# Kernel tuning notes

Measured on AMD Instinct MI355X. Metric: run time of the kernel, lower is better.

The kernel has to match this reference:

```python
import jax, jax.numpy as jnp
import numpy as np

S, T, BERT, POS = 256, 512, 768, 128
H1 = 1024
NUM_CLASSES = 6


def setup_inputs() -> dict:
    key = jax.random.key(0)
    ks = jax.random.split(key, 12)
    emb = jax.random.normal(ks[0], (S, T, BERT), dtype=jnp.float32)
    pos = jax.random.normal(ks[1], (S, T, POS), dtype=jnp.float32)
    seg = jnp.sort(jax.random.randint(ks[2], (S,), 0, 64)).astype(jnp.int32)
    scale = 0.02
    return {
        "embeddings": emb,
        "position_encodings": pos,
        "W_attn": jax.random.normal(ks[3], (BERT + POS, 1), dtype=jnp.float32) * scale,
        "b_attn": jnp.zeros((1,), dtype=jnp.float32),
        "W1": jax.random.normal(ks[4], (BERT, H1), dtype=jnp.float32) * scale,
        "b1": jnp.zeros((H1,), dtype=jnp.float32),
        "W2": jax.random.normal(ks[5], (H1, H1), dtype=jnp.float32) * scale,
        "b2": jnp.zeros((H1,), dtype=jnp.float32),
        "W3": jax.random.normal(ks[6], (H1, NUM_CLASSES), dtype=jnp.float32) * scale,
        "b3": jnp.zeros((NUM_CLASSES,), dtype=jnp.float32),
        "segment_ids": seg,
        "num_comments": 64,
    }


def reference(embeddings, position_encodings, W_attn, b_attn, W1, b1, W2, b2, W3, b3, segment_ids, num_comments):
    # attention logits: Linear(bert+pos -> 1) over concatenated features, shape (S, T, 1)
    attn = jnp.concatenate([embeddings, position_encodings], axis=2) @ W_attn + b_attn
    # per-segment softmax over the 512-token dim (torch Softmax(1) on (b-a, 512, 1))
    w = jax.nn.softmax(attn, axis=1)
    # softmax-weighted pooling per segment -> (S, BERT)
    segvec = jnp.sum(w * embeddings, axis=1)
    # ragged sum over each comment's segments (contiguous bounds == sorted segment ids)
    vecs = jax.ops.segment_sum(segvec, segment_ids, num_segments=num_comments)
    # MLP head with LeakyReLU (torch default slope 0.01) and Sigmoid
    h = jax.nn.leaky_relu(vecs @ W1 + b1, negative_slope=0.01)
    h = jax.nn.leaky_relu(h @ W2 + b2, negative_slope=0.01)
    return jax.nn.sigmoid(h @ W3 + b3)
```

## Files before the change

### kernel.cpp

```cpp
#include <hip/hip_runtime.h>
#include <math.h>

#define S_SEQ 256
#define T_TOK 512
#define BERT 768
#define POSD 128
#define H1 1024
#define NC 6

#define HALF_T 256
#define TILE_T 16
#define NTILES (HALF_T / TILE_T)

__global__ __launch_bounds__(256, 2) void pool_kernel(
    const float* __restrict__ emb, const float* __restrict__ pos,
    const float* __restrict__ Wa, const float* __restrict__ ba,
    float* __restrict__ part_acc, float* __restrict__ part_ml)
{
    __shared__ float lds_tile[TILE_T * BERT];
    __shared__ float lds_plog[HALF_T];
    __shared__ float lds_logit[TILE_T];

    const int tid  = threadIdx.x;
    const int wave = tid >> 6;
    const int lane = tid & 63;
    const int b    = blockIdx.x;
    const int s    = b >> 1;
    const int t0   = (b & 1) * HALF_T;

    const float4* Wa4 = (const float4*)Wa;
    float4 wa_e[3];
    wa_e[0] = Wa4[lane];
    wa_e[1] = Wa4[64 + lane];
    wa_e[2] = Wa4[128 + lane];
    const int lane32 = lane & 31;
    const int half32 = lane >> 5;
    const float4 wp = Wa4[192 + lane32];
    const float bav = ba[0];

    const float4* pos4 = (const float4*)pos;
    #pragma unroll 4
    for (int it = 0; it < 32; ++it) {
        const int tl = wave * 64 + it * 2 + half32;
        const size_t gi = ((size_t)s * T_TOK + (t0 + tl)) * (POSD/4) + lane32;
        const float4 p = pos4[gi];
        float d = p.x*wp.x + p.y*wp.y + p.z*wp.z + p.w*wp.w;
        #pragma unroll
        for (int off = 16; off >= 1; off >>= 1) d += __shfl_xor(d, off, 32);
        if (lane32 == 0) lds_plog[tl] = d + bav;
    }

    float m = -INFINITY;
    float l = 0.f;
    float acc0 = 0.f, acc1 = 0.f, acc2 = 0.f;

    const float4* emb_blk4 =
        (const float4*)(emb + ((size_t)s * T_TOK + t0) * BERT);
    float4* lds4 = (float4*)lds_tile;

    for (int tt = 0; tt < NTILES; ++tt) {
        __syncthreads();

        {
            const float4* src = emb_blk4 + (size_t)tt * (TILE_T*BERT/4);
            float4 tmp[12];
            #pragma unroll
            for (int i = 0; i < 12; ++i) tmp[i] = src[i*256 + tid];
            #pragma unroll
            for (int i = 0; i < 12; ++i) lds4[i*256 + tid] = tmp[i];
        }
        __syncthreads();

        #pragma unroll
        for (int q = 0; q < 4; ++q) {
            const int t = wave * 4 + q;
            const float4* row4 = (const float4*)&lds_tile[t * BERT];
            float d = 0.f;
            #pragma unroll
            for (int i = 0; i < 3; ++i) {
                const float4 v = row4[i*64 + lane];
                d += v.x*wa_e[i].x + v.y*wa_e[i].y + v.z*wa_e[i].z + v.w*wa_e[i].w;
            }
            #pragma unroll
            for (int off = 32; off >= 1; off >>= 1) d += __shfl_xor(d, off, 64);
            if (lane == 0) lds_logit[t] = d + lds_plog[tt*TILE_T + t];
        }
        __syncthreads();

        float tmax = lds_logit[0];
        #pragma unroll
        for (int t = 1; t < TILE_T; ++t) tmax = fmaxf(tmax, lds_logit[t]);
        const float m_new = fmaxf(m, tmax);
        const float alpha = __expf(m - m_new);
        float p[TILE_T];
        float psum = 0.f;
        #pragma unroll
        for (int t = 0; t < TILE_T; ++t) {
            p[t] = __expf(lds_logit[t] - m_new);
            psum += p[t];
        }
        l = l * alpha + psum;
        acc0 *= alpha; acc1 *= alpha; acc2 *= alpha;
        #pragma unroll
        for (int t = 0; t < TILE_T; ++t) {
            acc0 = fmaf(p[t], lds_tile[t*BERT +       tid], acc0);
            acc1 = fmaf(p[t], lds_tile[t*BERT + 256 + tid], acc1);
            acc2 = fmaf(p[t], lds_tile[t*BERT + 512 + tid], acc2);
        }
        m = m_new;
    }

    part_acc[(size_t)b*BERT +       tid] = acc0;
    part_acc[(size_t)b*BERT + 256 + tid] = acc1;
    part_acc[(size_t)b*BERT + 512 + tid] = acc2;
    if (tid == 0) { part_ml[b*2] = m; part_ml[b*2+1] = l; }
}

__global__ void combine_segsum(
    const float* __restrict__ part_acc, const float* __restrict__ part_ml,
    const int* __restrict__ seg, float* __restrict__ vecs)
{
    const int c = blockIdx.x;
    const int tid = threadIdx.x;
    float v0 = 0.f, v1 = 0.f, v2 = 0.f;
    for (int s = 0; s < S_SEQ; ++s) {
        if (seg[s] != c) continue;
        const int p0 = 2*s, p1 = 2*s + 1;
        const float m0 = part_ml[p0*2], l0 = part_ml[p0*2+1];
        const float m1 = part_ml[p1*2], l1 = part_ml[p1*2+1];
        const float M  = fmaxf(m0, m1);
        const float e0 = __expf(m0 - M), e1 = __expf(m1 - M);
        const float inv = 1.0f / (l0*e0 + l1*e1);
        const float a = e0 * inv, bb = e1 * inv;
        v0 += a*part_acc[(size_t)p0*BERT +       tid] + bb*part_acc[(size_t)p1*BERT +       tid];
        v1 += a*part_acc[(size_t)p0*BERT + 256 + tid] + bb*part_acc[(size_t)p1*BERT + 256 + tid];
        v2 += a*part_acc[(size_t)p0*BERT + 512 + tid] + bb*part_acc[(size_t)p1*BERT + 512 + tid];
    }
    vecs[(size_t)c*BERT +       tid] = v0;
    vecs[(size_t)c*BERT + 256 + tid] = v1;
    vecs[(size_t)c*BERT + 512 + tid] = v2;
}

__global__ void mlp_layer(
    const float* __restrict__ in, const float* __restrict__ W,
    const float* __restrict__ bias, float* __restrict__ out, int K)
{
    __shared__ float v[H1];
    const int c  = blockIdx.y;
    const int tid = threadIdx.x;
    const int j  = blockIdx.x * 256 + tid;
    for (int i = tid; i < K; i += 256) v[i] = in[(size_t)c*K + i];
    __syncthreads();
    float a0 = 0.f, a1 = 0.f, a2 = 0.f, a3 = 0.f;
    #pragma unroll 4
    for (int k = 0; k < K; k += 4) {
        a0 = fmaf(v[k  ], W[(size_t)(k  )*H1 + j], a0);
        a1 = fmaf(v[k+1], W[(size_t)(k+1)*H1 + j], a1);
        a2 = fmaf(v[k+2], W[(size_t)(k+2)*H1 + j], a2);
        a3 = fmaf(v[k+3], W[(size_t)(k+3)*H1 + j], a3);
    }
    const float acc = bias[j] + ((a0 + a1) + (a2 + a3));
    out[(size_t)c*H1 + j] = acc > 0.f ? acc : 0.01f * acc;
}

__global__ void mlp_out(
    const float* __restrict__ h, const float* __restrict__ W3,
    const float* __restrict__ b3, float* __restrict__ out)
{
    __shared__ float v[H1];
    __shared__ float red[NC][4];
    const int c = blockIdx.x;
    const int tid = threadIdx.x;
    const int wave = tid >> 6, lane = tid & 63;
    for (int i = tid; i < H1; i += 256) v[i] = h[(size_t)c*H1 + i];
    __syncthreads();
    float po[NC] = {0.f, 0.f, 0.f, 0.f, 0.f, 0.f};
    for (int k = tid; k < H1; k += 256) {
        const float hv = v[k];
        #pragma unroll
        for (int o = 0; o < NC; ++o) po[o] = fmaf(hv, W3[k*NC + o], po[o]);
    }
    #pragma unroll
    for (int o = 0; o < NC; ++o) {
        float d = po[o];
        #pragma unroll
        for (int off = 32; off >= 1; off >>= 1) d += __shfl_xor(d, off, 64);
        if (lane == 0) red[o][wave] = d;
    }
    __syncthreads();
    if (tid < NC) {
        const float sum = red[tid][0] + red[tid][1] + red[tid][2] + red[tid][3] + b3[tid];
        out[c*NC + tid] = 1.0f / (1.0f + __expf(-sum));
    }
}

extern "C" void kernel_launch(void* const* d_in, const int* in_sizes, int n_in,
                              void* d_out, int out_size, void* d_ws, size_t ws_size,
                              hipStream_t stream)
{
    const float* emb = (const float*)d_in[0];
    const float* pos = (const float*)d_in[1];
    const float* Wa  = (const float*)d_in[2];
    const float* ba  = (const float*)d_in[3];
    const float* W1  = (const float*)d_in[4];
    const float* b1  = (const float*)d_in[5];
    const float* W2  = (const float*)d_in[6];
    const float* b2  = (const float*)d_in[7];
    const float* W3  = (const float*)d_in[8];
    const float* b3  = (const float*)d_in[9];
    const int*   seg = (const int*)d_in[10];
    float* out = (float*)d_out;

    float* ws = (float*)d_ws;
    float* part_acc = ws;
    float* part_ml  = part_acc + 512*BERT;
    float* vecs     = part_ml  + 512*2;
    float* h1       = vecs     + 64*BERT;
    float* h2       = h1       + 64*H1;

    pool_kernel<<<512, 256, 0, stream>>>(emb, pos, Wa, ba, part_acc, part_ml);
    combine_segsum<<<64, 256, 0, stream>>>(part_acc, part_ml, seg, vecs);
    mlp_layer<<<dim3(4, 64), 256, 0, stream>>>(vecs, W1, b1, h1, BERT);
    mlp_layer<<<dim3(4, 64), 256, 0, stream>>>(h1, W2, b2, h2, H1);
    mlp_out<<<64, 256, 0, stream>>>(h2, W3, b3, out);
}
```

Before: 684.3 us.

## Double-buffer async LDS loads in pooling and batch comments in MLP layers

The pooling kernel splits each sequence into four 128-token chunks and streams 8-token tiles into LDS with async global-to-LDS loads, double-buffered so the next tile loads while the current one is processed. Each wave owns two tokens per tile and keeps per-lane accumulators, and an online-softmax merge across waves replaces the per-tile block barriers and serial logit scan. The combine step is updated to merge four partials per sequence. The MLP layers now process four comments per block so each weight load is reused four times. Costs include more partial traffic and possible LDS bank conflicts from the strided per-lane row reads.

Measured after the change: 812.2 us. 18.7% more time.

```diff
diff --git a/kernel.cpp b/kernel.cpp
--- a/kernel.cpp
+++ b/kernel.cpp
@@ -1,5 +1,6 @@
 #include <hip/hip_runtime.h>
 #include <math.h>
+#include <stdint.h>
 
 #define S_SEQ 256
 #define T_TOK 512
@@ -8,112 +9,139 @@
 #define H1 1024
 #define NC 6
 
-#define HALF_T 256
-#define TILE_T 16
-#define NTILES (HALF_T / TILE_T)
-
-__global__ __launch_bounds__(256, 2) void pool_kernel(
+#define CHUNK_T 128
+#define TILE_T 8
+#define NTILES (CHUNK_T / TILE_T)
+#define TILE_FLOATS (TILE_T * BERT)
+
+__device__ __forceinline__ void async_load16(const float* g, float* lds_uniform) {
+    auto* l3 = reinterpret_cast<__attribute__((address_space(3))) uint32_t*>(
+        reinterpret_cast<uintptr_t>(lds_uniform));
+    auto* g1 = reinterpret_cast<const __attribute__((address_space(1))) uint32_t*>(
+        reinterpret_cast<uintptr_t>(g));
+    __builtin_amdgcn_global_load_lds(g1, l3, 16, 0, 0);
+}
+
+__global__ __launch_bounds__(256, 3) void pool_kernel(
     const float* __restrict__ emb, const float* __restrict__ pos,
     const float* __restrict__ Wa, const float* __restrict__ ba,
     float* __restrict__ part_acc, float* __restrict__ part_ml)
 {
-    __shared__ float lds_tile[TILE_T * BERT];
-    __shared__ float lds_plog[HALF_T];
-    __shared__ float lds_logit[TILE_T];
-
-    const int tid  = threadIdx.x;
-    const int wave = tid >> 6;
-    const int lane = tid & 63;
-    const int b    = blockIdx.x;
-    const int s    = b >> 1;
-    const int t0   = (b & 1) * HALF_T;
+    __shared__ float smem[2 * TILE_FLOATS + CHUNK_T + 8];
+    float* plog = smem + 2 * TILE_FLOATS;
+    float* wml  = plog + CHUNK_T;
+
+    const int tid = threadIdx.x;
+    const int w   = tid >> 6;
+    const int l   = tid & 63;
+    const int b   = blockIdx.x;
+    const int s   = b >> 2;
+    const int t0  = (b & 3) * CHUNK_T;
+
+    const float* gbase = emb + ((size_t)s * T_TOK + t0) * BERT;
+
+    #pragma unroll
+    for (int c = 0; c < 6; ++c)
+        async_load16(gbase + (w * 6 + c) * 256 + l * 4, smem + (w * 6 + c) * 256);
 
     const float4* Wa4 = (const float4*)Wa;
-    float4 wa_e[3];
-    wa_e[0] = Wa4[lane];
-    wa_e[1] = Wa4[64 + lane];
-    wa_e[2] = Wa4[128 + lane];
-    const int lane32 = lane & 31;
-    const int half32 = lane >> 5;
-    const float4 wp = Wa4[192 + lane32];
+    const float4 wa0 = Wa4[l * 3 + 0];
+    const float4 wa1 = Wa4[l * 3 + 1];
+    const float4 wa2 = Wa4[l * 3 + 2];
+    const int l32 = l & 31;
+    const float4 wp = Wa4[192 + l32];
     const float bav = ba[0];
 
     const float4* pos4 = (const float4*)pos;
-    #pragma unroll 4
-    for (int it = 0; it < 32; ++it) {
-        const int tl = wave * 64 + it * 2 + half32;
-        const size_t gi = ((size_t)s * T_TOK + (t0 + tl)) * (POSD/4) + lane32;
-        const float4 p = pos4[gi];
-        float d = p.x*wp.x + p.y*wp.y + p.z*wp.z + p.w*wp.w;
+    const int hw = tid >> 5;
+    for (int it = 0; it < CHUNK_T / 8; ++it) {
+        const int tl = it * 8 + hw;
+        const float4 p = pos4[((size_t)s * T_TOK + t0 + tl) * (POSD / 4) + l32];
+        float d = p.x * wp.x + p.y * wp.y + p.z * wp.z + p.w * wp.w;
         #pragma unroll
         for (int off = 16; off >= 1; off >>= 1) d += __shfl_xor(d, off, 32);
-        if (lane32 == 0) lds_plog[tl] = d + bav;
-    }
-
-    float m = -INFINITY;
-    float l = 0.f;
-    float acc0 = 0.f, acc1 = 0.f, acc2 = 0.f;
-
-    const float4* emb_blk4 =
-        (const float4*)(emb + ((size_t)s * T_TOK + t0) * BERT);
-    float4* lds4 = (float4*)lds_tile;
+        if (l32 == 0) plog[tl] = d + bav;
+    }
+
+    float m = -INFINITY, lsum = 0.f;
+    float acc[12];
+    #pragma unroll
+    for (int j = 0; j < 12; ++j) acc[j] = 0.f;
 
     for (int tt = 0; tt < NTILES; ++tt) {
+        float* cur = smem + (tt & 1) * TILE_FLOATS;
         __syncthreads();
 
-        {
-            const float4* src = emb_blk4 + (size_t)tt * (TILE_T*BERT/4);
-            float4 tmp[12];
+        if (tt + 1 < NTILES) {
+            float* nxt = smem + ((tt + 1) & 1) * TILE_FLOATS;
+            const float* src = gbase + (size_t)(tt + 1) * TILE_FLOATS;
             #pragma unroll
-            for (int i = 0; i < 12; ++i) tmp[i] = src[i*256 + tid];
-            #pragma unroll
-            for (int i = 0; i < 12; ++i) lds4[i*256 + tid] = tmp[i];
+            for (int c = 0; c < 6; ++c)
+                async_load16(src + (w * 6 + c) * 256 + l * 4, nxt + (w * 6 + c) * 256);
         }
-        __syncthreads();
-
-        #pragma unroll
-        for (int q = 0; q < 4; ++q) {
-            const int t = wave * 4 + q;
-            const float4* row4 = (const float4*)&lds_tile[t * BERT];
-            float d = 0.f;
-            #pragma unroll
-            for (int i = 0; i < 3; ++i) {
-                const float4 v = row4[i*64 + lane];
-                d += v.x*wa_e[i].x + v.y*wa_e[i].y + v.z*wa_e[i].z + v.w*wa_e[i].w;
-            }
-            #pragma unroll
-            for (int off = 32; off >= 1; off >>= 1) d += __shfl_xor(d, off, 64);
-            if (lane == 0) lds_logit[t] = d + lds_plog[tt*TILE_T + t];
+
+        const int i0 = tt * TILE_T + w * 2;
+        const float4* r0 = (const float4*)(cur + (w * 2) * BERT);
+        const float4* r1 = (const float4*)(cur + (w * 2 + 1) * BERT);
+        const float4 a0 = r0[l * 3 + 0], a1 = r0[l * 3 + 1], a2 = r0[l * 3 + 2];
+        const float4 b0 = r1[l * 3 + 0], b1 = r1[l * 3 + 1], b2 = r1[l * 3 + 2];
+
+        float d0 = a0.x*wa0.x + a0.y*wa0.y + a0.z*wa0.z + a0.w*wa0.w
+                 + a1.x*wa1.x + a1.y*wa1.y + a1.z*wa1.z + a1.w*wa1.w
+                 + a2.x*wa2.x + a2.y*wa2.y + a2.z*wa2.z + a2.w*wa2.w;
+        float d1 = b0.x*wa0.x + b0.y*wa0.y + b0.z*wa0.z + b0.w*wa0.w
+                 + b1.x*wa1.x + b1.y*wa1.y + b1.z*wa1.z + b1.w*wa1.w
+                 + b2.x*wa2.x + b2.y*wa2.y + b2.z*wa2.z + b2.w*wa2.w;
+        #pragma unroll
+        for (int off = 32; off >= 1; off >>= 1) {
+            d0 += __shfl_xor(d0, off, 64);
+            d1 += __shfl_xor(d1, off, 64);
         }
-        __syncthreads();
-
-        float tmax = lds_logit[0];
-        #pragma unroll
-        for (int t = 1; t < TILE_T; ++t) tmax = fmaxf(tmax, lds_logit[t]);
-        const float m_new = fmaxf(m, tmax);
-        const float alpha = __expf(m - m_new);
-        float p[TILE_T];
-        float psum = 0.f;
-        #pragma unroll
-        for (int t = 0; t < TILE_T; ++t) {
-            p[t] = __expf(lds_logit[t] - m_new);
-            psum += p[t];
-        }
-        l = l * alpha + psum;
-        acc0 *= alpha; acc1 *= alpha; acc2 *= alpha;
-        #pragma unroll
-        for (int t = 0; t < TILE_T; ++t) {
-            acc0 = fmaf(p[t], lds_tile[t*BERT +       tid], acc0);
-            acc1 = fmaf(p[t], lds_tile[t*BERT + 256 + tid], acc1);
-            acc2 = fmaf(p[t], lds_tile[t*BERT + 512 + tid], acc2);
-        }
-        m = m_new;
-    }
-
-    part_acc[(size_t)b*BERT +       tid] = acc0;
-    part_acc[(size_t)b*BERT + 256 + tid] = acc1;
-    part_acc[(size_t)b*BERT + 512 + tid] = acc2;
-    if (tid == 0) { part_ml[b*2] = m; part_ml[b*2+1] = l; }
+
+        const float lg0 = d0 + plog[i0];
+        const float lg1 = d1 + plog[i0 + 1];
+        const float mn = fmaxf(m, fmaxf(lg0, lg1));
+        const float alpha = __expf(m - mn);
+        const float p0 = __expf(lg0 - mn);
+        const float p1 = __expf(lg1 - mn);
+        lsum = lsum * alpha + p0 + p1;
+        m = mn;
+
+        acc[0]  = fmaf(p0, a0.x, fmaf(p1, b0.x, acc[0]  * alpha));
+        acc[1]  = fmaf(p0, a0.y, fmaf(p1, b0.y, acc[1]  * alpha));
+        acc[2]  = fmaf(p0, a0.z, fmaf(p1, b0.z, acc[2]  * alpha));
+        acc[3]  = fmaf(p0, a0.w, fmaf(p1, b0.w, acc[3]  * alpha));
+        acc[4]  = fmaf(p0, a1.x, fmaf(p1, b1.x, acc[4]  * alpha));
+        acc[5]  = fmaf(p0, a1.y, fmaf(p1, b1.y, acc[5]  * alpha));
+        acc[6]  = fmaf(p0, a1.z, fmaf(p1, b1.z, acc[6]  * alpha));
+        acc[7]  = fmaf(p0, a1.w, fmaf(p1, b1.w, acc[7]  * alpha));
+        acc[8]  = fmaf(p0, a2.x, fmaf(p1, b2.x, acc[8]  * alpha));
+        acc[9]  = fmaf(p0, a2.y, fmaf(p1, b2.y, acc[9]  * alpha));
+        acc[10] = fmaf(p0, a2.z, fmaf(p1, b2.z, acc[10] * alpha));
+        acc[11] = fmaf(p0, a2.w, fmaf(p1, b2.w, acc[11] * alpha));
+    }
+
+    __syncthreads();
+    float* mg = smem;
+    #pragma unroll
+    for (int j = 0; j < 12; ++j) mg[w * BERT + l * 12 + j] = acc[j];
+    if (l == 0) { wml[w * 2] = m; wml[w * 2 + 1] = lsum; }
+    __syncthreads();
+
+    const float m0 = wml[0], l0 = wml[1], m1 = wml[2], l1 = wml[3];
+    const float m2 = wml[4], l2 = wml[5], m3 = wml[6], l3 = wml[7];
+    const float M  = fmaxf(fmaxf(m0, m1), fmaxf(m2, m3));
+    const float e0 = __expf(m0 - M), e1 = __expf(m1 - M);
+    const float e2 = __expf(m2 - M), e3 = __expf(m3 - M);
+    const float lt = l0 * e0 + l1 * e1 + l2 * e2 + l3 * e3;
+    #pragma unroll
+    for (int k = 0; k < 3; ++k) {
+        const int col = tid * 3 + k;
+        const float v = e0 * mg[col] + e1 * mg[BERT + col]
+                      + e2 * mg[2 * BERT + col] + e3 * mg[3 * BERT + col];
+        part_acc[(size_t)b * BERT + col] = v;
+    }
+    if (tid == 0) { part_ml[b * 2] = M; part_ml[b * 2 + 1] = lt; }
 }
 
 __global__ void combine_segsum(
@@ -125,42 +153,59 @@
     float v0 = 0.f, v1 = 0.f, v2 = 0.f;
     for (int s = 0; s < S_SEQ; ++s) {
         if (seg[s] != c) continue;
-        const int p0 = 2*s, p1 = 2*s + 1;
-        const float m0 = part_ml[p0*2], l0 = part_ml[p0*2+1];
-        const float m1 = part_ml[p1*2], l1 = part_ml[p1*2+1];
-        const float M  = fmaxf(m0, m1);
+        const int p = s * 4;
+        const float m0 = part_ml[(p+0)*2], l0 = part_ml[(p+0)*2+1];
+        const float m1 = part_ml[(p+1)*2], l1 = part_ml[(p+1)*2+1];
+        const float m2 = part_ml[(p+2)*2], l2 = part_ml[(p+2)*2+1];
+        const float m3 = part_ml[(p+3)*2], l3 = part_ml[(p+3)*2+1];
+        const float M  = fmaxf(fmaxf(m0, m1), fmaxf(m2, m3));
         const float e0 = __expf(m0 - M), e1 = __expf(m1 - M);
-        const float inv = 1.0f / (l0*e0 + l1*e1);
-        const float a = e0 * inv, bb = e1 * inv;
-        v0 += a*part_acc[(size_t)p0*BERT +       tid] + bb*part_acc[(size_t)p1*BERT +       tid];
-        v1 += a*part_acc[(size_t)p0*BERT + 256 + tid] + bb*part_acc[(size_t)p1*BERT + 256 + tid];
-        v2 += a*part_acc[(size_t)p0*BERT + 512 + tid] + bb*part_acc[(size_t)p1*BERT + 512 + tid];
-    }
-    vecs[(size_t)c*BERT +       tid] = v0;
-    vecs[(size_t)c*BERT + 256 + tid] = v1;
-    vecs[(size_t)c*BERT + 512 + tid] = v2;
+        const float e2 = __expf(m2 - M), e3 = __expf(m3 - M);
+        const float inv = 1.0f / (l0*e0 + l1*e1 + l2*e2 + l3*e3);
+        const int col = tid * 3;
+        v0 += inv * (e0 * part_acc[(size_t)(p+0)*BERT + col]
+                   + e1 * part_acc[(size_t)(p+1)*BERT + col]
+                   + e2 * part_acc[(size_t)(p+2)*BERT + col]
+                   + e3 * part_acc[(size_t)(p+3)*BERT + col]);
+        v1 += inv * (e0 * part_acc[(size_t)(p+0)*BERT + col + 1]
+                   + e1 * part_acc[(size_t)(p+1)*BERT + col + 1]
+                   + e2 * part_acc[(size_t)(p+2)*BERT + col + 1]
+                   + e3 * part_acc[(size_t)(p+3)*BERT + col + 1]);
+        v2 += inv * (e0 * part_acc[(size_t)(p+0)*BERT + col + 2]
+                   + e1 * part_acc[(size_t)(p+1)*BERT + col + 2]
+                   + e2 * part_acc[(size_t)(p+2)*BERT + col + 2]
+                   + e3 * part_acc[(size_t)(p+3)*BERT + col + 2]);
+    }
+    vecs[(size_t)c*BERT + tid*3 + 0] = v0;
+    vecs[(size_t)c*BERT + tid*3 + 1] = v1;
+    vecs[(size_t)c*BERT + tid*3 + 2] = v2;
 }
 
 __global__ void mlp_layer(
     const float* __restrict__ in, const float* __restrict__ W,
     const float* __restrict__ bias, float* __restrict__ out, int K)
 {
-    __shared__ float v[H1];
-    const int c  = blockIdx.y;
-    const int tid = threadIdx.x;
-    const int j  = blockIdx.x * 256 + tid;
-    for (int i = tid; i < K; i += 256) v[i] = in[(size_t)c*K + i];
+    __shared__ float vf[4 * H1];
+    const int tid = threadIdx.x;
+    const int c0  = blockIdx.y * 4;
+    const int j   = blockIdx.x * 256 + tid;
+    for (int i = tid; i < 4 * K; i += 256) vf[i] = in[(size_t)c0 * K + i];
     __syncthreads();
     float a0 = 0.f, a1 = 0.f, a2 = 0.f, a3 = 0.f;
     #pragma unroll 4
-    for (int k = 0; k < K; k += 4) {
-        a0 = fmaf(v[k  ], W[(size_t)(k  )*H1 + j], a0);
-        a1 = fmaf(v[k+1], W[(size_t)(k+1)*H1 + j], a1);
-        a2 = fmaf(v[k+2], W[(size_t)(k+2)*H1 + j], a2);
-        a3 = fmaf(v[k+3], W[(size_t)(k+3)*H1 + j], a3);
-    }
-    const float acc = bias[j] + ((a0 + a1) + (a2 + a3));
-    out[(size_t)c*H1 + j] = acc > 0.f ? acc : 0.01f * acc;
+    for (int k = 0; k < K; ++k) {
+        const float wv = W[(size_t)k * H1 + j];
+        a0 = fmaf(vf[k],         wv, a0);
+        a1 = fmaf(vf[K + k],     wv, a1);
+        a2 = fmaf(vf[2 * K + k], wv, a2);
+        a3 = fmaf(vf[3 * K + k], wv, a3);
+    }
+    const float bj = bias[j];
+    float r;
+    r = a0 + bj; out[(size_t)(c0+0)*H1 + j] = r > 0.f ? r : 0.01f * r;
+    r = a1 + bj; out[(size_t)(c0+1)*H1 + j] = r > 0.f ? r : 0.01f * r;
+    r = a2 + bj; out[(size_t)(c0+2)*H1 + j] = r > 0.f ? r : 0.01f * r;
+    r = a3 + bj; out[(size_t)(c0+3)*H1 + j] = r > 0.f ? r : 0.01f * r;
 }
 
 __global__ void mlp_out(
@@ -172,13 +217,13 @@
     const int c = blockIdx.x;
     const int tid = threadIdx.x;
     const int wave = tid >> 6, lane = tid & 63;
-    for (int i = tid; i < H1; i += 256) v[i] = h[(size_t)c*H1 + i];
+    for (int i = tid; i < H1; i += 256) v[i] = h[(size_t)c * H1 + i];
     __syncthreads();
     float po[NC] = {0.f, 0.f, 0.f, 0.f, 0.f, 0.f};
     for (int k = tid; k < H1; k += 256) {
         const float hv = v[k];
         #pragma unroll
-        for (int o = 0; o < NC; ++o) po[o] = fmaf(hv, W3[k*NC + o], po[o]);
+        for (int o = 0; o < NC; ++o) po[o] = fmaf(hv, W3[k * NC + o], po[o]);
     }
     #pragma unroll
     for (int o = 0; o < NC; ++o) {
@@ -190,7 +235,7 @@
     __syncthreads();
     if (tid < NC) {
         const float sum = red[tid][0] + red[tid][1] + red[tid][2] + red[tid][3] + b3[tid];
-        out[c*NC + tid] = 1.0f / (1.0f + __expf(-sum));
+        out[c * NC + tid] = 1.0f / (1.0f + __expf(-sum));
     }
 }
 
@@ -213,14 +258,14 @@
 
     float* ws = (float*)d_ws;
     float* part_acc = ws;
-    float* part_ml  = part_acc + 512*BERT;
-    float* vecs     = part_ml  + 512*2;
-    float* h1       = vecs     + 64*BERT;
-    float* h2       = h1       + 64*H1;
-
-    pool_kernel<<<512, 256, 0, stream>>>(emb, pos, Wa, ba, part_acc, part_ml);
+    float* part_ml  = part_acc + 1024 * BERT;
+    float* vecs     = part_ml  + 1024 * 2;
+    float* h1       = vecs     + 64 * BERT;
+    float* h2       = h1       + 64 * H1;
+
+    pool_kernel<<<1024, 256, 0, stream>>>(emb, pos, Wa, ba, part_acc, part_ml);
     combine_segsum<<<64, 256, 0, stream>>>(part_acc, part_ml, seg, vecs);
-    mlp_layer<<<dim3(4, 64), 256, 0, stream>>>(vecs, W1, b1, h1, BERT);
-    mlp_layer<<<dim3(4, 64), 256, 0, stream>>>(h1, W2, b2, h2, H1);
+    mlp_layer<<<dim3(4, 16), 256, 0, stream>>>(vecs, W1, b1, h1, BERT);
+    mlp_layer<<<dim3(4, 16), 256, 0, stream>>>(h1, W2, b2, h2, H1);
     mlp_out<<<64, 256, 0, stream>>>(h2, W3, b3, out);
 }
```
